# Performance work log

Measured on AMD Instinct MI355X. Metric: run time of the kernel, lower is better.

## Reference

```python
import jax, jax.numpy as jnp
import numpy as np

B, T = 32, 64
STOCH, DETER, HIDDEN = 1024, 4096, 1024
ACT_DIM, EMBED = 128, 1536
MIN_STD = 0.1
EPS = 1e-3  # dreamerv3-torch uses LayerNorm(eps=1e-3)


def _ln(x, g, b):
    m = jnp.mean(x, -1, keepdims=True)
    v = jnp.var(x, -1, keepdims=True)
    return (x - m) * jax.lax.rsqrt(v + EPS) * g + b


def setup_inputs() -> dict:
    key = jax.random.key(0)
    ks = jax.random.split(key, 24)

    def w(k, fan_in, fan_out):
        return jax.random.normal(k, (fan_in, fan_out), jnp.float32) / np.sqrt(fan_in)

    inp = {
        "embed": jax.random.normal(ks[0], (B, T, EMBED), jnp.float32),
        "action": jax.random.normal(ks[1], (B, T, ACT_DIM), jnp.float32),
        "is_first": jnp.zeros((B, T), jnp.bool_),
        "init_deter": jax.random.normal(ks[2], (B, DETER), jnp.float32),
        "init_stoch": jax.random.normal(ks[3], (B, STOCH), jnp.float32),
        "noise_prior": jax.random.normal(ks[4], (B, T, STOCH), jnp.float32),
        "noise_post": jax.random.normal(ks[5], (B, T, STOCH), jnp.float32),
        # _img_in_layers: Linear(stoch+act -> hidden, no bias) + LN + SiLU
        "W_in": w(ks[6], STOCH + ACT_DIM, HIDDEN),
        "g_in": 1.0 + 0.1 * jax.random.normal(ks[7], (HIDDEN,), jnp.float32),
        "b_in": 0.1 * jax.random.normal(ks[8], (HIDDEN,), jnp.float32),
        # GRUCell: Linear(hidden+deter -> 3*deter, no bias) + LN
        "W_gru": w(ks[9], HIDDEN + DETER, 3 * DETER),
        "g_gru": 1.0 + 0.1 * jax.random.normal(ks[10], (3 * DETER,), jnp.float32),
        "b_gru": 0.1 * jax.random.normal(ks[11], (3 * DETER,), jnp.float32),
        # _img_out_layers: Linear(deter -> hidden, no bias) + LN + SiLU
        "W_imgout": w(ks[12], DETER, HIDDEN),
        "g_io": 1.0 + 0.1 * jax.random.normal(ks[13], (HIDDEN,), jnp.float32),
        "b_io": 0.1 * jax.random.normal(ks[14], (HIDDEN,), jnp.float32),
        # _obs_out_layers: Linear(deter+embed -> hidden, no bias) + LN + SiLU
        "W_obsout": w(ks[15], DETER + EMBED, HIDDEN),
        "g_oo": 1.0 + 0.1 * jax.random.normal(ks[16], (HIDDEN,), jnp.float32),
        "b_oo": 0.1 * jax.random.normal(ks[17], (HIDDEN,), jnp.float32),
        # suff-stats layers: Linear(hidden -> 2*stoch) with bias
        "W_ims": w(ks[18], HIDDEN, 2 * STOCH),
        "b_ims": 0.01 * jax.random.normal(ks[19], (2 * STOCH,), jnp.float32),
        "W_obs": w(ks[20], HIDDEN, 2 * STOCH),
        "b_obs": 0.01 * jax.random.normal(ks[21], (2 * STOCH,), jnp.float32),
    }
    return inp


def _observe(embed, action, init_deter, init_stoch, noise_prior, noise_post,
             W_in, g_in, b_in, W_gru, g_gru, b_gru, W_imgout, g_io, b_io,
             W_obsout, g_oo, b_oo, W_ims, b_ims, W_obs, b_obs):
    def suff_stats(h, W, b, noise):
        stats = h @ W + b
        mean, std = jnp.split(stats, 2, -1)
        std = jax.nn.softplus(std) + MIN_STD  # std_act='softplus', mean_act='none'
        return mean, std, mean + std * noise

    def step(carry, xs):
        deter, stoch = carry
        e, a, n_p, n_q = xs
        # img_in: concat(prev_stoch, action) -> Linear -> LN -> SiLU
        x = jax.nn.silu(_ln(jnp.concatenate([stoch, a], -1) @ W_in, g_in, b_in))
        # GRUCell with layernorm (update_bias = -1)
        parts = _ln(jnp.concatenate([x, deter], -1) @ W_gru, g_gru, b_gru)
        reset, cand, update = jnp.split(parts, 3, -1)
        reset = jax.nn.sigmoid(reset)
        cand = jnp.tanh(reset * cand)
        update = jax.nn.sigmoid(update - 1.0)
        deter = update * cand + (1.0 - update) * deter
        # prior (imagination) suff stats + sample
        h_p = jax.nn.silu(_ln(deter @ W_imgout, g_io, b_io))
        mean_p, std_p, stoch_p = suff_stats(h_p, W_ims, b_ims, n_p)
        # posterior (observation) suff stats + sample
        h_q = jax.nn.silu(_ln(jnp.concatenate([deter, e], -1) @ W_obsout, g_oo, b_oo))
        mean_q, std_q, stoch_q = suff_stats(h_q, W_obs, b_obs, n_q)
        out = jnp.concatenate([deter, stoch_q, mean_q, std_q, stoch_p, mean_p, std_p], -1)
        return (deter, stoch_q), out

    xs = (jnp.swapaxes(embed, 0, 1), jnp.swapaxes(action, 0, 1),
          jnp.swapaxes(noise_prior, 0, 1), jnp.swapaxes(noise_post, 0, 1))
    _, outs = jax.lax.scan(step, (init_deter, init_stoch), xs)
    return jnp.swapaxes(outs, 0, 1)  # [B, T, deter + 6*stoch]


def reference(embed, action, is_first, init_deter, init_stoch, noise_prior, noise_post,
              W_in, g_in, b_in, W_gru, g_gru, b_gru, W_imgout, g_io, b_io,
              W_obsout, g_oo, b_oo, W_ims, b_ims, W_obs, b_obs):
    # is_first is all-False and state is given, so the init-mixing branch is never taken
    del is_first
    return _observe(embed, action, init_deter, init_stoch, noise_prior, noise_post,
                    W_in, g_in, b_in, W_gru, g_gru, b_gru, W_imgout, g_io, b_io,
                    W_obsout, g_oo, b_oo, W_ims, b_ims, W_obs, b_obs)
```

## Files before the change

kernel.cpp:

```cpp
#include <hip/hip_runtime.h>
#include <hip/hip_bf16.h>

#define B_ 32
#define T_ 64
#define STOCH_ 1024
#define DETER_ 4096
#define HID_ 1024
#define EMB_ 1536
#define ACTD_ 128
#define GRUK 5120
#define GRUN 12288
#define KC 512
#define LDAP (KC + 8)

typedef __attribute__((ext_vector_type(8))) __bf16 bf16x8;
typedef __attribute__((ext_vector_type(4))) float f32x4;
typedef __attribute__((ext_vector_type(8))) unsigned short u16x8;
typedef __attribute__((ext_vector_type(4))) unsigned short u16x4;

__device__ inline unsigned short f2bf(float f) {
    union { float f; unsigned u; } x; x.f = f;
    unsigned r = x.u + 0x7fffu + ((x.u >> 16) & 1u);
    return (unsigned short)(r >> 16);
}
__device__ inline float sigmoidf_(float v) { return 1.f / (1.f + __expf(-v)); }
__device__ inline float siluf_(float v)    { return v / (1.f + __expf(-v)); }
__device__ inline float softplusf_(float v){ return fmaxf(v, 0.f) + __logf(1.f + __expf(-fabsf(v))); }


__global__ __launch_bounds__(256) void k_pack(const float* __restrict__ W,
                                              unsigned short* __restrict__ dst,
                                              int K, int N) {
    long fid = (long)blockIdx.x * 256 + threadIdx.x;
    long nfr = (long)K * N / 8;
    if (fid >= nfr) return;
    int lane = (int)(fid & 63);
    long tile = fid >> 6;
    int ktiles = K >> 5;
    int k_t = (int)(tile % ktiles);
    int n_t = (int)(tile / ktiles);
    int c = lane & 15, kb = lane >> 4;
    int k0 = k_t * 32 + kb * 8;
    int n = n_t * 16 + c;
    unsigned short v[8];
#pragma unroll
    for (int i = 0; i < 8; i++) v[i] = f2bf(W[(long)(k0 + i) * N + n]);
    *reinterpret_cast<u16x8*>(dst + fid * 8) = *reinterpret_cast<u16x8*>(v);
}

__global__ __launch_bounds__(256) void k_conv(const float* __restrict__ s,
                                              unsigned short* __restrict__ d, long n) {
    long i = ((long)blockIdx.x * 256 + threadIdx.x) * 4;
    if (i >= n) return;
    f32x4 v = *reinterpret_cast<const f32x4*>(s + i);
    unsigned short o[4];
#pragma unroll
    for (int k = 0; k < 4; k++) o[k] = f2bf(v[k]);
    *reinterpret_cast<u16x4*>(d + i) = *reinterpret_cast<u16x4*>(o);
}

__global__ __launch_bounds__(256) void k_copy(const float* __restrict__ s,
                                              float* __restrict__ d, long n) {
    long i = ((long)blockIdx.x * 256 + threadIdx.x) * 4;
    if (i >= n) return;
    *reinterpret_cast<f32x4*>(d + i) = *reinterpret_cast<const f32x4*>(s + i);
}


__device__ inline void ln_stats_prologue(const float* __restrict__ partials, int nslab,
                                         float invN, float* s_mean, float* s_rstd) {
    if (threadIdx.x < 32) {
        int r = threadIdx.x;
        float s = 0.f, q = 0.f;
        for (int j = 0; j < nslab; j++) {
            s += partials[((long)j * 32 + r) * 2];
            q += partials[((long)j * 32 + r) * 2 + 1];
        }
        float m = s * invN;
        float var = q * invN - m * m;
        s_mean[r] = m;
        s_rstd[r] = rsqrtf(var + 1e-3f);
    }
    __syncthreads();
}

__device__ inline void stage_bf16(unsigned short* __restrict__ lds_a,
                                  const unsigned short* __restrict__ src,
                                  int lda, int k0, int cw) {
    for (int e = (int)threadIdx.x * 8; e < 32 * cw; e += 256 * 8) {
        int row = e / cw, col = e - row * cw;
        *reinterpret_cast<u16x8*>(&lds_a[row * LDAP + col]) =
            *reinterpret_cast<const u16x8*>(&src[(long)row * lda + k0 + col]);
    }
}

__device__ inline void stage_lnsilu(unsigned short* __restrict__ lds_a,
                                    const float* __restrict__ raw, int ldr, int colbase,
                                    int k0, int cw,
                                    const float* __restrict__ g, const float* __restrict__ b,
                                    const float* s_mean, const float* s_rstd) {
    for (int e = (int)threadIdx.x * 8; e < 32 * cw; e += 256 * 8) {
        int row = e / cw, col = e - row * cw;
        int kg = k0 + col;
        float m = s_mean[row], rs = s_rstd[row];
        const float* sp = &raw[(long)row * ldr + colbase + kg];
        unsigned short v[8];
#pragma unroll
        for (int i = 0; i < 8; i++) {
            float ln = (sp[i] - m) * rs * g[kg + i] + b[kg + i];
            v[i] = f2bf(siluf_(ln));
        }
        *reinterpret_cast<u16x8*>(&lds_a[row * LDAP + col]) = *reinterpret_cast<u16x8*>(v);
    }
}

__device__ inline void mfma_chunk(const unsigned short* __restrict__ lds_a,
                                  const unsigned short* __restrict__ Bp,
                                  int ntile, long Ktiles, long kt0, int nkt,
                                  int lane, f32x4& acc0, f32x4& acc1) {
    int c = lane & 15, kb = lane >> 4;
    const unsigned short* a0p = &lds_a[c * LDAP + kb * 8];
    const unsigned short* a1p = &lds_a[(16 + c) * LDAP + kb * 8];
    const unsigned short* bp = Bp + ((long)ntile * Ktiles + kt0) * 512 + lane * 8;
    for (int kt = 0; kt < nkt; ++kt) {
        bf16x8 a0 = *reinterpret_cast<const bf16x8*>(a0p + kt * 32);
        bf16x8 a1 = *reinterpret_cast<const bf16x8*>(a1p + kt * 32);
        bf16x8 bv = *reinterpret_cast<const bf16x8*>(bp + (long)kt * 512);
        acc0 = __builtin_amdgcn_mfma_f32_16x16x32_bf16(a0, bv, acc0, 0, 0, 0);
        acc1 = __builtin_amdgcn_mfma_f32_16x16x32_bf16(a1, bv, acc1, 0, 0, 0);
    }
}

__device__ inline void acc_to_lds(float (*s_out)[66], int wave, int lane,
                                  const f32x4& acc0, const f32x4& acc1) {
    int c = lane & 15, rb = lane >> 4;
#pragma unroll
    for (int j = 0; j < 4; j++) {
        s_out[rb * 4 + j][wave * 16 + c] = acc0[j];
        s_out[16 + rb * 4 + j][wave * 16 + c] = acc1[j];
    }
}

__device__ inline void epi_raw(float (*s_out)[66],
                               const float* __restrict__ addin, long addin_ld, int n0_add,
                               float* __restrict__ outp, long out_ld, int n0_out,
                               float* __restrict__ partials, int slab) {
    int row = threadIdx.x >> 3, c8 = (threadIdx.x & 7) * 8;
    float vals[8];
#pragma unroll
    for (int i = 0; i < 8; i++) {
        float v = s_out[row][c8 + i];
        if (addin) v += addin[(long)row * addin_ld + n0_add + c8 + i];
        vals[i] = v;
        s_out[row][c8 + i] = v;
    }
#pragma unroll
    for (int i = 0; i < 8; i++) outp[(long)row * out_ld + n0_out + c8 + i] = vals[i];
    __syncthreads();
    if (threadIdx.x < 32) {
        float s = 0.f, q = 0.f;
        for (int j = 0; j < 64; j++) { float v = s_out[threadIdx.x][j]; s += v; q += v * v; }
        partials[((long)slab * 32 + threadIdx.x) * 2] = s;
        partials[((long)slab * 32 + threadIdx.x) * 2 + 1] = q;
    }
}


__global__ __launch_bounds__(256) void k_x(const unsigned short* __restrict__ Bp,
                                           const unsigned short* __restrict__ stoch_bf16,
                                           const float* __restrict__ A_pre_t,
                                           float* __restrict__ x_raw, float* __restrict__ px) {
    __shared__ __align__(16) unsigned short lds_a[32 * LDAP];
    __shared__ float s_out[32][66];
    int wave = threadIdx.x >> 6, lane = threadIdx.x & 63;
    int ntile = blockIdx.x * 4 + wave;
    f32x4 acc0 = {0.f, 0.f, 0.f, 0.f}, acc1 = {0.f, 0.f, 0.f, 0.f};
    for (int ch = 0; ch < 2; ++ch) {
        __syncthreads();
        stage_bf16(lds_a, stoch_bf16, STOCH_, ch * KC, KC);
        __syncthreads();
        mfma_chunk(lds_a, Bp, ntile, 32, ch * 16, 16, lane, acc0, acc1);
    }
    __syncthreads();
    acc_to_lds(s_out, wave, lane, acc0, acc1);
    __syncthreads();
    epi_raw(s_out, A_pre_t, (long)T_ * 1024, blockIdx.x * 64,
            x_raw, 1024, blockIdx.x * 64, px, blockIdx.x);
}

__global__ __launch_bounds__(256) void k_gru(const unsigned short* __restrict__ Bp,
                                             const float* __restrict__ x_raw,
                                             const float* __restrict__ px,
                                             const float* __restrict__ g_in,
                                             const float* __restrict__ b_in,
                                             const unsigned short* __restrict__ deter_bf16,
                                             float* __restrict__ G_raw, float* __restrict__ pg) {
    __shared__ __align__(16) unsigned short lds_a[32 * LDAP];
    __shared__ float s_out[32][66];
    __shared__ float s_mean[32], s_rstd[32];
    ln_stats_prologue(px, 16, 1.f / 1024.f, s_mean, s_rstd);
    int wave = threadIdx.x >> 6, lane = threadIdx.x & 63;
    int ntile = blockIdx.x * 4 + wave;
    f32x4 acc0 = {0.f, 0.f, 0.f, 0.f}, acc1 = {0.f, 0.f, 0.f, 0.f};
    for (int ch = 0; ch < 10; ++ch) {
        __syncthreads();
        if (ch < 2) stage_lnsilu(lds_a, x_raw, 1024, 0, ch * KC, KC, g_in, b_in, s_mean, s_rstd);
        else        stage_bf16(lds_a, deter_bf16, DETER_, ch * KC - 1024, KC);
        __syncthreads();
        mfma_chunk(lds_a, Bp, ntile, 160, ch * 16, 16, lane, acc0, acc1);
    }
    __syncthreads();
    acc_to_lds(s_out, wave, lane, acc0, acc1);
    __syncthreads();
    epi_raw(s_out, nullptr, 0, 0, G_raw, GRUN, blockIdx.x * 64, pg, blockIdx.x);
}

__global__ __launch_bounds__(256) void k_deter(const float* __restrict__ G_raw,
                                               const float* __restrict__ pg,
                                               const float* __restrict__ g_gru,
                                               const float* __restrict__ b_gru,
                                               float* __restrict__ deter_f32,
                                               unsigned short* __restrict__ deter_bf16,
                                               float* __restrict__ out, int t) {
    __shared__ float s_mean[32], s_rstd[32];
    ln_stats_prologue(pg, 192, 1.f / 12288.f, s_mean, s_rstd);
    int eid = blockIdx.x * 256 + threadIdx.x;
    int b = eid >> 10;
    int j = (eid & 1023) * 4;
    const float* gr = G_raw + (long)b * GRUN;
    f32x4 r4 = *reinterpret_cast<const f32x4*>(gr + j);
    f32x4 c4 = *reinterpret_cast<const f32x4*>(gr + 4096 + j);
    f32x4 u4 = *reinterpret_cast<const f32x4*>(gr + 8192 + j);
    f32x4 d4 = *reinterpret_cast<const f32x4*>(deter_f32 + (long)b * DETER_ + j);
    float m = s_mean[b], rs = s_rstd[b];
    f32x4 nd;
    unsigned short db[4];
#pragma unroll
    for (int i = 0; i < 4; i++) {
        float lr = (r4[i] - m) * rs * g_gru[j + i] + b_gru[j + i];
        float lc = (c4[i] - m) * rs * g_gru[4096 + j + i] + b_gru[4096 + j + i];
        float lu = (u4[i] - m) * rs * g_gru[8192 + j + i] + b_gru[8192 + j + i];
        float reset = sigmoidf_(lr);
        float cand = tanhf(reset * lc);
        float upd = sigmoidf_(lu - 1.f);
        float dn = upd * cand + (1.f - upd) * d4[i];
        nd[i] = dn; db[i] = f2bf(dn);
    }
    *reinterpret_cast<f32x4*>(deter_f32 + (long)b * DETER_ + j) = nd;
    *reinterpret_cast<u16x4*>(deter_bf16 + (long)b * DETER_ + j) = *reinterpret_cast<u16x4*>(db);
    *reinterpret_cast<f32x4*>(out + ((long)(b * T_ + t)) * 10240 + j) = nd;
}

__global__ __launch_bounds__(256) void k_h(const unsigned short* __restrict__ Wio,
                                           const unsigned short* __restrict__ Wood,
                                           const unsigned short* __restrict__ deter_bf16,
                                           const float* __restrict__ E_pre_t,
                                           float* __restrict__ h_raw, float* __restrict__ ph) {
    __shared__ __align__(16) unsigned short lds_a[32 * LDAP];
    __shared__ float s_out[32][66];
    int p = blockIdx.x < 16;
    int bi = blockIdx.x & 15;
    const unsigned short* Bp = p ? Wio : Wood;
    int wave = threadIdx.x >> 6, lane = threadIdx.x & 63;
    int ntile = bi * 4 + wave;
    f32x4 acc0 = {0.f, 0.f, 0.f, 0.f}, acc1 = {0.f, 0.f, 0.f, 0.f};
    for (int ch = 0; ch < 8; ++ch) {
        __syncthreads();
        stage_bf16(lds_a, deter_bf16, DETER_, ch * KC, KC);
        __syncthreads();
        mfma_chunk(lds_a, Bp, ntile, 128, ch * 16, 16, lane, acc0, acc1);
    }
    __syncthreads();
    acc_to_lds(s_out, wave, lane, acc0, acc1);
    __syncthreads();
    epi_raw(s_out, p ? nullptr : E_pre_t, (long)T_ * 1024, bi * 64,
            h_raw, 2048, (p ? 0 : 1024) + bi * 64, ph, blockIdx.x);
}

__global__ __launch_bounds__(256) void k_stats(const unsigned short* __restrict__ Wims,
                                               const unsigned short* __restrict__ Wobs,
                                               const float* __restrict__ h_raw,
                                               const float* __restrict__ ph,
                                               const float* __restrict__ g_io,
                                               const float* __restrict__ b_io,
                                               const float* __restrict__ g_oo,
                                               const float* __restrict__ b_oo,
                                               const float* __restrict__ b_ims,
                                               const float* __restrict__ b_obs,
                                               const float* __restrict__ noise_p,
                                               const float* __restrict__ noise_q,
                                               float* __restrict__ out,
                                               unsigned short* __restrict__ stoch_bf16, int t) {
    __shared__ __align__(16) unsigned short lds_a[32 * LDAP];
    __shared__ float s_out[32][66];
    __shared__ float s_mean[32], s_rstd[32];
    int q = blockIdx.x >= 32;
    int s = blockIdx.x & 31;
    ln_stats_prologue(ph + (q ? 16 * 32 * 2 : 0), 16, 1.f / 1024.f, s_mean, s_rstd);
    const unsigned short* Bp = q ? Wobs : Wims;
    const float* g = q ? g_oo : g_io;
    const float* bb = q ? b_oo : b_io;
    const float* bias = q ? b_obs : b_ims;
    int colbase = q ? 1024 : 0;
    int wave = threadIdx.x >> 6, lane = threadIdx.x & 63;
    int ntile = (wave < 2) ? (s * 2 + wave) : (64 + s * 2 + (wave - 2));
    f32x4 acc0 = {0.f, 0.f, 0.f, 0.f}, acc1 = {0.f, 0.f, 0.f, 0.f};
    for (int ch = 0; ch < 2; ++ch) {
        __syncthreads();
        stage_lnsilu(lds_a, h_raw, 2048, colbase, ch * KC, KC, g, bb, s_mean, s_rstd);
        __syncthreads();
        mfma_chunk(lds_a, Bp, ntile, 32, ch * 16, 16, lane, acc0, acc1);
    }
    __syncthreads();
    int c = lane & 15, rb = lane >> 4;
    float bv = bias[ntile * 16 + c];
#pragma unroll
    for (int j = 0; j < 4; j++) {
        s_out[rb * 4 + j][wave * 16 + c] = acc0[j] + bv;
        s_out[16 + rb * 4 + j][wave * 16 + c] = acc1[j] + bv;
    }
    __syncthreads();
    int r = threadIdx.x >> 3, j0 = (threadIdx.x & 7) * 4;
    const float* noise = q ? noise_q : noise_p;
#pragma unroll
    for (int i = 0; i < 4; i++) {
        int jj = j0 + i;
        float mean = s_out[r][jj];
        float sv = s_out[r][32 + jj];
        float sd = softplusf_(sv) + 0.1f;
        int cg = s * 32 + jj;
        float nz = noise[((long)(r * T_ + t)) * 1024 + cg];
        float st = mean + sd * nz;
        float* orow = out + ((long)(r * T_ + t)) * 10240;
        if (q) {
            orow[4096 + cg] = st; orow[5120 + cg] = mean; orow[6144 + cg] = sd;
            stoch_bf16[(long)r * 1024 + cg] = f2bf(st);
        } else {
            orow[7168 + cg] = st; orow[8192 + cg] = mean; orow[9216 + cg] = sd;
        }
    }
}

__global__ __launch_bounds__(256) void k_prepgemm(const unsigned short* __restrict__ A, int K,
                                                  const unsigned short* __restrict__ Bp,
                                                  float* __restrict__ outp) {
    __shared__ __align__(16) unsigned short lds_a[32 * LDAP];
    __shared__ float s_out[32][66];
    int wave = threadIdx.x >> 6, lane = threadIdx.x & 63;
    int ntile = blockIdx.x * 4 + wave;
    int m0 = blockIdx.y * 32;
    int Ktiles = K >> 5;
    f32x4 acc0 = {0.f, 0.f, 0.f, 0.f}, acc1 = {0.f, 0.f, 0.f, 0.f};
    int nch = (K + KC - 1) / KC;
    for (int ch = 0; ch < nch; ++ch) {
        int cw = K - ch * KC; if (cw > KC) cw = KC;
        __syncthreads();
        stage_bf16(lds_a, A + (long)m0 * K, K, ch * KC, cw);
        __syncthreads();
        mfma_chunk(lds_a, Bp, ntile, Ktiles, ch * 16, cw >> 5, lane, acc0, acc1);
    }
    __syncthreads();
    acc_to_lds(s_out, wave, lane, acc0, acc1);
    __syncthreads();
    int row = threadIdx.x >> 3, c8 = (threadIdx.x & 7) * 8;
#pragma unroll
    for (int i = 0; i < 8; i++)
        outp[(long)(m0 + row) * 1024 + blockIdx.x * 64 + c8 + i] = s_out[row][c8 + i];
}


extern "C" void kernel_launch(void* const* d_in, const int* in_sizes, int n_in,
                              void* d_out, int out_size, void* d_ws, size_t ws_size,
                              hipStream_t stream) {
    const float* embed      = (const float*)d_in[0];
    const float* action     = (const float*)d_in[1];
    const float* init_deter = (const float*)d_in[3];
    const float* init_stoch = (const float*)d_in[4];
    const float* noise_pr   = (const float*)d_in[5];
    const float* noise_po   = (const float*)d_in[6];
    const float* W_in       = (const float*)d_in[7];
    const float* g_in       = (const float*)d_in[8];
    const float* b_in       = (const float*)d_in[9];
    const float* W_gru      = (const float*)d_in[10];
    const float* g_gru      = (const float*)d_in[11];
    const float* b_gru      = (const float*)d_in[12];
    const float* W_io       = (const float*)d_in[13];
    const float* g_io       = (const float*)d_in[14];
    const float* b_io       = (const float*)d_in[15];
    const float* W_oo       = (const float*)d_in[16];
    const float* g_oo       = (const float*)d_in[17];
    const float* b_oo       = (const float*)d_in[18];
    const float* W_ims      = (const float*)d_in[19];
    const float* b_ims      = (const float*)d_in[20];
    const float* W_obs      = (const float*)d_in[21];
    const float* b_obs      = (const float*)d_in[22];
    float* out = (float*)d_out;

    char* ws = (char*)d_ws;
    size_t off = 0;
    auto alloc = [&](size_t bytes) {
        size_t r = off;
        off = (off + bytes + 255) & ~(size_t)255;
        return r;
    };
    unsigned short* pWgru  = (unsigned short*)(ws + alloc((size_t)GRUK * GRUN * 2));
    unsigned short* pWin_s = (unsigned short*)(ws + alloc((size_t)1024 * 1024 * 2));
    unsigned short* pWin_a = (unsigned short*)(ws + alloc((size_t)128 * 1024 * 2));
    unsigned short* pWio   = (unsigned short*)(ws + alloc((size_t)4096 * 1024 * 2));
    unsigned short* pWood  = (unsigned short*)(ws + alloc((size_t)4096 * 1024 * 2));
    unsigned short* pWooe  = (unsigned short*)(ws + alloc((size_t)1536 * 1024 * 2));
    unsigned short* pWims  = (unsigned short*)(ws + alloc((size_t)1024 * 2048 * 2));
    unsigned short* pWobs  = (unsigned short*)(ws + alloc((size_t)1024 * 2048 * 2));
    unsigned short* act_bf = (unsigned short*)(ws + alloc((size_t)2048 * 128 * 2));
    unsigned short* emb_bf = (unsigned short*)(ws + alloc((size_t)2048 * 1536 * 2));
    float* A_pre  = (float*)(ws + alloc((size_t)2048 * 1024 * 4));
    float* E_pre  = (float*)(ws + alloc((size_t)2048 * 1024 * 4));
    float* x_raw  = (float*)(ws + alloc((size_t)32 * 1024 * 4));
    float* G_raw  = (float*)(ws + alloc((size_t)32 * GRUN * 4));
    float* h_raw  = (float*)(ws + alloc((size_t)32 * 2048 * 4));
    float* deterf = (float*)(ws + alloc((size_t)32 * DETER_ * 4));
    unsigned short* deterb = (unsigned short*)(ws + alloc((size_t)32 * DETER_ * 2));
    unsigned short* stochb = (unsigned short*)(ws + alloc((size_t)32 * 1024 * 2));
    float* px = (float*)(ws + alloc((size_t)16 * 32 * 2 * 4));
    float* pg = (float*)(ws + alloc((size_t)192 * 32 * 2 * 4));
    float* ph = (float*)(ws + alloc((size_t)32 * 32 * 2 * 4));
    (void)ws_size; (void)out_size; (void)n_in; (void)in_sizes;

    auto packgrid = [](long K, long N) { return (unsigned)((K * N / 8 + 255) / 256); };

    k_pack<<<packgrid(5120, 12288), 256, 0, stream>>>(W_gru, pWgru, 5120, 12288);
    k_pack<<<packgrid(1024, 1024), 256, 0, stream>>>(W_in, pWin_s, 1024, 1024);
    k_pack<<<packgrid(128, 1024), 256, 0, stream>>>(W_in + (size_t)1024 * 1024, pWin_a, 128, 1024);
    k_pack<<<packgrid(4096, 1024), 256, 0, stream>>>(W_io, pWio, 4096, 1024);
    k_pack<<<packgrid(4096, 1024), 256, 0, stream>>>(W_oo, pWood, 4096, 1024);
    k_pack<<<packgrid(1536, 1024), 256, 0, stream>>>(W_oo + (size_t)4096 * 1024, pWooe, 1536, 1024);
    k_pack<<<packgrid(1024, 2048), 256, 0, stream>>>(W_ims, pWims, 1024, 2048);
    k_pack<<<packgrid(1024, 2048), 256, 0, stream>>>(W_obs, pWobs, 1024, 2048);
    k_conv<<<(2048 * 128 / 4 + 255) / 256, 256, 0, stream>>>(action, act_bf, 2048L * 128);
    k_conv<<<(2048 * 1536 / 4 + 255) / 256, 256, 0, stream>>>(embed, emb_bf, 2048L * 1536);
    k_conv<<<(32 * 1024 / 4 + 255) / 256, 256, 0, stream>>>(init_stoch, stochb, 32L * 1024);
    k_conv<<<(32 * 4096 / 4 + 255) / 256, 256, 0, stream>>>(init_deter, deterb, 32L * 4096);
    k_copy<<<(32 * 4096 / 4 + 255) / 256, 256, 0, stream>>>(init_deter, deterf, 32L * 4096);
    k_prepgemm<<<dim3(16, 64), 256, 0, stream>>>(act_bf, 128, pWin_a, A_pre);
    k_prepgemm<<<dim3(16, 64), 256, 0, stream>>>(emb_bf, 1536, pWooe, E_pre);

    for (int t = 0; t < T_; ++t) {
        k_x<<<16, 256, 0, stream>>>(pWin_s, stochb, A_pre + (size_t)t * 1024, x_raw, px);
        k_gru<<<192, 256, 0, stream>>>(pWgru, x_raw, px, g_in, b_in, deterb, G_raw, pg);
        k_deter<<<128, 256, 0, stream>>>(G_raw, pg, g_gru, b_gru, deterf, deterb, out, t);
        k_h<<<32, 256, 0, stream>>>(pWio, pWood, deterb, E_pre + (size_t)t * 1024, h_raw, ph);
        k_stats<<<64, 256, 0, stream>>>(pWims, pWobs, h_raw, ph, g_io, b_io, g_oo, b_oo,
                                        b_ims, b_obs, noise_pr, noise_po, out, stochb, t);
    }
}
```

Measured before the change: 7.235 ms.

## Hoist prior branch out of recurrence and pipeline GEMMs with async LDS loads

The prior-path computation (img_out layer and prior suff stats) does not feed the recurrence, so it moves out of the per-step loop. Each step's deter is saved to a bf16 buffer, and the prior branch then runs as one batched GEMM over all 2048 rows after the loop. The per-step GEMMs are unified into a templated kernel. It double-buffers A tiles in LDS using global_load_lds with an XOR swizzle, and uses smaller 32-column N tiles so more blocks run. The GRU candidate also switches to a fast exp-based tanh, which trades a little accuracy and adds a 16 MB buffer for the saved deter history.

```diff
diff --git a/kernel.cpp b/kernel.cpp
--- a/kernel.cpp
+++ b/kernel.cpp
@@ -1,17 +1,9 @@
 #include <hip/hip_runtime.h>
 #include <hip/hip_bf16.h>
 
-#define B_ 32
 #define T_ 64
-#define STOCH_ 1024
 #define DETER_ 4096
-#define HID_ 1024
-#define EMB_ 1536
-#define ACTD_ 128
-#define GRUK 5120
 #define GRUN 12288
-#define KC 512
-#define LDAP (KC + 8)
 
 typedef __attribute__((ext_vector_type(8))) __bf16 bf16x8;
 typedef __attribute__((ext_vector_type(4))) float f32x4;
@@ -26,6 +18,19 @@
 __device__ inline float sigmoidf_(float v) { return 1.f / (1.f + __expf(-v)); }
 __device__ inline float siluf_(float v)    { return v / (1.f + __expf(-v)); }
 __device__ inline float softplusf_(float v){ return fmaxf(v, 0.f) + __logf(1.f + __expf(-fabsf(v))); }
+__device__ inline float tanhf_(float v)    { return 2.f / (1.f + __expf(-2.f * v)) - 1.f; }
+
+__device__ inline void barrier_() {
+    asm volatile("" ::: "memory");
+    __builtin_amdgcn_s_barrier();
+    asm volatile("" ::: "memory");
+}
+template <int N> __device__ inline void vmwaitN() {
+    asm volatile("s_waitcnt vmcnt(%0)" :: "i"(N) : "memory");
+}
+__device__ inline void lgkmwait_() {
+    asm volatile("s_waitcnt lgkmcnt(0)" ::: "memory");
+}
 
 
 __global__ __launch_bounds__(256) void k_pack(const float* __restrict__ W,
@@ -67,152 +72,137 @@
 }
 
 
-__device__ inline void ln_stats_prologue(const float* __restrict__ partials, int nslab,
-                                         float invN, float* s_mean, float* s_rstd) {
-    if (threadIdx.x < 32) {
-        int r = threadIdx.x;
-        float s = 0.f, q = 0.f;
-        for (int j = 0; j < nslab; j++) {
-            s += partials[((long)j * 32 + r) * 2];
-            q += partials[((long)j * 32 + r) * 2 + 1];
+template <int CW>
+__device__ inline void stage_glds(unsigned short* chunk, const unsigned short* __restrict__ src,
+                                  long ld, long k0) {
+    constexpr int NI = (32 * CW * 2) / 4096;
+    int wv = (int)threadIdx.x >> 6, lane = (int)threadIdx.x & 63;
+#pragma unroll
+    for (int i = 0; i < NI; ++i) {
+        int obase = (wv * NI + i) << 10;
+        int o = obase + lane * 16;
+        int row = o / (CW * 2);
+        int cb = o - row * (CW * 2);
+        int gb = cb ^ ((row & 7) << 4);
+        const char* ga = (const char*)(src + (long)row * ld + k0) + gb;
+        __builtin_amdgcn_global_load_lds(
+            (const __attribute__((address_space(1))) void*)ga,
+            (__attribute__((address_space(3))) void*)(chunk + (obase >> 1)),
+            16, 0, 0);
+    }
+}
+
+__device__ inline void stage_ln512(unsigned short* chunk, const float* __restrict__ raw,
+                                   int ld, int col0,
+                                   const float* __restrict__ g, const float* __restrict__ b,
+                                   const float* s_mean, const float* s_rstd) {
+    int tid = threadIdx.x;
+#pragma unroll
+    for (int i = 0; i < 8; ++i) {
+        int e = tid * 8 + i * 2048;
+        int row = e >> 9, col = e & 511;
+        float m = s_mean[row], rs = s_rstd[row];
+        const float* sp = raw + (long)row * ld + col0 + col;
+        unsigned short pk[8];
+#pragma unroll
+        for (int j = 0; j < 8; ++j) {
+            float ln = (sp[j] - m) * rs * g[col0 + col + j] + b[col0 + col + j];
+            pk[j] = f2bf(siluf_(ln));
         }
-        float m = s * invN;
-        float var = q * invN - m * m;
-        s_mean[r] = m;
-        s_rstd[r] = rsqrtf(var + 1e-3f);
-    }
-    __syncthreads();
-}
-
-__device__ inline void stage_bf16(unsigned short* __restrict__ lds_a,
-                                  const unsigned short* __restrict__ src,
-                                  int lda, int k0, int cw) {
-    for (int e = (int)threadIdx.x * 8; e < 32 * cw; e += 256 * 8) {
-        int row = e / cw, col = e - row * cw;
-        *reinterpret_cast<u16x8*>(&lds_a[row * LDAP + col]) =
-            *reinterpret_cast<const u16x8*>(&src[(long)row * lda + k0 + col]);
-    }
-}
-
-__device__ inline void stage_lnsilu(unsigned short* __restrict__ lds_a,
-                                    const float* __restrict__ raw, int ldr, int colbase,
-                                    int k0, int cw,
-                                    const float* __restrict__ g, const float* __restrict__ b,
-                                    const float* s_mean, const float* s_rstd) {
-    for (int e = (int)threadIdx.x * 8; e < 32 * cw; e += 256 * 8) {
-        int row = e / cw, col = e - row * cw;
-        int kg = k0 + col;
-        float m = s_mean[row], rs = s_rstd[row];
-        const float* sp = &raw[(long)row * ldr + colbase + kg];
-        unsigned short v[8];
-#pragma unroll
-        for (int i = 0; i < 8; i++) {
-            float ln = (sp[i] - m) * rs * g[kg + i] + b[kg + i];
-            v[i] = f2bf(siluf_(ln));
+        int dcol = col ^ ((row & 7) << 3);
+        *reinterpret_cast<u16x8*>(chunk + row * 512 + dcol) = *reinterpret_cast<u16x8*>(pk);
+    }
+}
+
+template <int CW>
+__device__ inline void mfma_rh(const unsigned short* chunk, int row, int kb,
+                               const unsigned short* __restrict__ bp, f32x4& acc) {
+    constexpr int NKT = CW / 32;
+    const unsigned short* ap = chunk + row * CW;
+    int sw = (row & 7) << 3;
+#pragma unroll
+    for (int kt = 0; kt < NKT; ++kt) {
+        bf16x8 a = *reinterpret_cast<const bf16x8*>(ap + ((kb * 8 + kt * 32) ^ sw));
+        bf16x8 b = *reinterpret_cast<const bf16x8*>(bp + (long)kt * 512);
+        acc = __builtin_amdgcn_mfma_f32_16x16x32_bf16(a, b, acc, 0, 0, 0);
+    }
+}
+
+template <int CW, int NG, int NL>
+__global__ __launch_bounds__(256) void k_gemm32(
+    const unsigned short* __restrict__ Bp, int Ktiles, int ktg0,
+    const unsigned short* __restrict__ srcA, long ldA,
+    const float* __restrict__ lnraw, int lnld,
+    const float* __restrict__ g_ln, const float* __restrict__ b_ln,
+    const float* __restrict__ pstats, int nslab_in,
+    const float* __restrict__ addin, long addin_ld,
+    float* __restrict__ outp, long out_ld,
+    float* __restrict__ partials, long prows)
+{
+    constexpr int NCH = NG + NL;
+    constexpr int NI = (32 * CW * 2) / 4096;
+    __shared__ __align__(16) unsigned short sb[2][32 * CW];
+    __shared__ float s_out[32][34];
+    __shared__ float s_mean[32], s_rstd[32];
+    int tid = threadIdx.x;
+    if (NL > 0) {
+        if (tid < 32) {
+            float s = 0.f, q = 0.f;
+            for (int j = 0; j < nslab_in; ++j) {
+                s += pstats[((long)j * 32 + tid) * 2];
+                q += pstats[((long)j * 32 + tid) * 2 + 1];
+            }
+            float m = s * (1.f / 1024.f);
+            s_mean[tid] = m;
+            s_rstd[tid] = rsqrtf(q * (1.f / 1024.f) - m * m + 1e-3f);
         }
-        *reinterpret_cast<u16x8*>(&lds_a[row * LDAP + col]) = *reinterpret_cast<u16x8*>(v);
-    }
-}
-
-__device__ inline void mfma_chunk(const unsigned short* __restrict__ lds_a,
-                                  const unsigned short* __restrict__ Bp,
-                                  int ntile, long Ktiles, long kt0, int nkt,
-                                  int lane, f32x4& acc0, f32x4& acc1) {
+        __syncthreads();
+    }
+    int rowbase = blockIdx.y * 32;
+    const unsigned short* srcAr = srcA + (long)rowbase * ldA;
+    int lane = tid & 63, wv = tid >> 6;
+    int nt = wv >> 1, rh = wv & 1;
     int c = lane & 15, kb = lane >> 4;
-    const unsigned short* a0p = &lds_a[c * LDAP + kb * 8];
-    const unsigned short* a1p = &lds_a[(16 + c) * LDAP + kb * 8];
-    const unsigned short* bp = Bp + ((long)ntile * Ktiles + kt0) * 512 + lane * 8;
-    for (int kt = 0; kt < nkt; ++kt) {
-        bf16x8 a0 = *reinterpret_cast<const bf16x8*>(a0p + kt * 32);
-        bf16x8 a1 = *reinterpret_cast<const bf16x8*>(a1p + kt * 32);
-        bf16x8 bv = *reinterpret_cast<const bf16x8*>(bp + (long)kt * 512);
-        acc0 = __builtin_amdgcn_mfma_f32_16x16x32_bf16(a0, bv, acc0, 0, 0, 0);
-        acc1 = __builtin_amdgcn_mfma_f32_16x16x32_bf16(a1, bv, acc1, 0, 0, 0);
-    }
-}
-
-__device__ inline void acc_to_lds(float (*s_out)[66], int wave, int lane,
-                                  const f32x4& acc0, const f32x4& acc1) {
-    int c = lane & 15, rb = lane >> 4;
-#pragma unroll
-    for (int j = 0; j < 4; j++) {
-        s_out[rb * 4 + j][wave * 16 + c] = acc0[j];
-        s_out[16 + rb * 4 + j][wave * 16 + c] = acc1[j];
-    }
-}
-
-__device__ inline void epi_raw(float (*s_out)[66],
-                               const float* __restrict__ addin, long addin_ld, int n0_add,
-                               float* __restrict__ outp, long out_ld, int n0_out,
-                               float* __restrict__ partials, int slab) {
-    int row = threadIdx.x >> 3, c8 = (threadIdx.x & 7) * 8;
-    float vals[8];
-#pragma unroll
-    for (int i = 0; i < 8; i++) {
-        float v = s_out[row][c8 + i];
-        if (addin) v += addin[(long)row * addin_ld + n0_add + c8 + i];
-        vals[i] = v;
-        s_out[row][c8 + i] = v;
-    }
-#pragma unroll
-    for (int i = 0; i < 8; i++) outp[(long)row * out_ld + n0_out + c8 + i] = vals[i];
-    __syncthreads();
-    if (threadIdx.x < 32) {
-        float s = 0.f, q = 0.f;
-        for (int j = 0; j < 64; j++) { float v = s_out[threadIdx.x][j]; s += v; q += v * v; }
-        partials[((long)slab * 32 + threadIdx.x) * 2] = s;
-        partials[((long)slab * 32 + threadIdx.x) * 2 + 1] = q;
-    }
-}
-
-
-__global__ __launch_bounds__(256) void k_x(const unsigned short* __restrict__ Bp,
-                                           const unsigned short* __restrict__ stoch_bf16,
-                                           const float* __restrict__ A_pre_t,
-                                           float* __restrict__ x_raw, float* __restrict__ px) {
-    __shared__ __align__(16) unsigned short lds_a[32 * LDAP];
-    __shared__ float s_out[32][66];
-    int wave = threadIdx.x >> 6, lane = threadIdx.x & 63;
-    int ntile = blockIdx.x * 4 + wave;
-    f32x4 acc0 = {0.f, 0.f, 0.f, 0.f}, acc1 = {0.f, 0.f, 0.f, 0.f};
-    for (int ch = 0; ch < 2; ++ch) {
-        __syncthreads();
-        stage_bf16(lds_a, stoch_bf16, STOCH_, ch * KC, KC);
-        __syncthreads();
-        mfma_chunk(lds_a, Bp, ntile, 32, ch * 16, 16, lane, acc0, acc1);
-    }
-    __syncthreads();
-    acc_to_lds(s_out, wave, lane, acc0, acc1);
-    __syncthreads();
-    epi_raw(s_out, A_pre_t, (long)T_ * 1024, blockIdx.x * 64,
-            x_raw, 1024, blockIdx.x * 64, px, blockIdx.x);
-}
-
-__global__ __launch_bounds__(256) void k_gru(const unsigned short* __restrict__ Bp,
-                                             const float* __restrict__ x_raw,
-                                             const float* __restrict__ px,
-                                             const float* __restrict__ g_in,
-                                             const float* __restrict__ b_in,
-                                             const unsigned short* __restrict__ deter_bf16,
-                                             float* __restrict__ G_raw, float* __restrict__ pg) {
-    __shared__ __align__(16) unsigned short lds_a[32 * LDAP];
-    __shared__ float s_out[32][66];
-    __shared__ float s_mean[32], s_rstd[32];
-    ln_stats_prologue(px, 16, 1.f / 1024.f, s_mean, s_rstd);
-    int wave = threadIdx.x >> 6, lane = threadIdx.x & 63;
-    int ntile = blockIdx.x * 4 + wave;
-    f32x4 acc0 = {0.f, 0.f, 0.f, 0.f}, acc1 = {0.f, 0.f, 0.f, 0.f};
-    for (int ch = 0; ch < 10; ++ch) {
-        __syncthreads();
-        if (ch < 2) stage_lnsilu(lds_a, x_raw, 1024, 0, ch * KC, KC, g_in, b_in, s_mean, s_rstd);
-        else        stage_bf16(lds_a, deter_bf16, DETER_, ch * KC - 1024, KC);
-        __syncthreads();
-        mfma_chunk(lds_a, Bp, ntile, 160, ch * 16, 16, lane, acc0, acc1);
-    }
-    __syncthreads();
-    acc_to_lds(s_out, wave, lane, acc0, acc1);
-    __syncthreads();
-    epi_raw(s_out, nullptr, 0, 0, G_raw, GRUN, blockIdx.x * 64, pg, blockIdx.x);
+    int mrow = rh * 16 + c;
+    long ntg = (long)blockIdx.x * 2 + nt;
+    const unsigned short* bbase = Bp + (long)ntg * Ktiles * 512 + lane * 8;
+    f32x4 acc = {0.f, 0.f, 0.f, 0.f};
+    stage_glds<CW>(sb[0], srcAr, ldA, 0);
+    for (int ch = 0; ch < NCH; ++ch) {
+        int nx = ch + 1;
+        if (nx < NG) stage_glds<CW>(sb[nx & 1], srcAr, ldA, (long)nx * CW);
+        else if (nx < NCH) stage_ln512(sb[nx & 1], lnraw, lnld, (nx - NG) * 512,
+                                       g_ln, b_ln, s_mean, s_rstd);
+        if (ch < NG) { if (nx < NG) vmwaitN<NI>(); else vmwaitN<0>(); }
+        if (nx >= NG && nx < NCH) lgkmwait_();
+        barrier_();
+        int kt0 = (ch < NG) ? (ktg0 + ch * (CW / 32)) : ((ch - NG) * 16);
+        mfma_rh<CW>(sb[ch & 1], mrow, kb, bbase + (long)kt0 * 512, acc);
+        barrier_();
+    }
+    __syncthreads();
+#pragma unroll
+    for (int j = 0; j < 4; ++j) s_out[rh * 16 + kb * 4 + j][nt * 16 + c] = acc[j];
+    __syncthreads();
+    int orow = tid >> 3, c4 = (tid & 7) * 4;
+    long rg = rowbase + orow;
+    float v[4]; float s = 0.f, q = 0.f;
+#pragma unroll
+    for (int i = 0; i < 4; ++i) {
+        float x = s_out[orow][c4 + i];
+        if (addin) x += addin[rg * addin_ld + blockIdx.x * 32 + c4 + i];
+        v[i] = x; s += x; q += x * x;
+    }
+#pragma unroll
+    for (int i = 0; i < 4; ++i) outp[rg * out_ld + blockIdx.x * 32 + c4 + i] = v[i];
+    if (partials) {
+#pragma unroll
+        for (int m = 1; m < 8; m <<= 1) { s += __shfl_xor(s, m); q += __shfl_xor(q, m); }
+        if ((tid & 7) == 0) {
+            partials[((long)blockIdx.x * prows + rg) * 2] = s;
+            partials[((long)blockIdx.x * prows + rg) * 2 + 1] = q;
+        }
+    }
 }
 
 __global__ __launch_bounds__(256) void k_deter(const float* __restrict__ G_raw,
@@ -221,10 +211,31 @@
                                                const float* __restrict__ b_gru,
                                                float* __restrict__ deter_f32,
                                                unsigned short* __restrict__ deter_bf16,
+                                               unsigned short* __restrict__ deter_allb,
                                                float* __restrict__ out, int t) {
     __shared__ float s_mean[32], s_rstd[32];
-    ln_stats_prologue(pg, 192, 1.f / 12288.f, s_mean, s_rstd);
-    int eid = blockIdx.x * 256 + threadIdx.x;
+    __shared__ float s_red[2][8][32];
+    int tid = threadIdx.x;
+    {
+        int r = tid & 31, g = tid >> 5;
+        float s = 0.f, q = 0.f;
+        for (int j = g; j < 384; j += 8) {
+            s += pg[((long)j * 32 + r) * 2];
+            q += pg[((long)j * 32 + r) * 2 + 1];
+        }
+        s_red[0][g][r] = s; s_red[1][g][r] = q;
+    }
+    __syncthreads();
+    if (tid < 32) {
+        float s = 0.f, q = 0.f;
+#pragma unroll
+        for (int g = 0; g < 8; ++g) { s += s_red[0][g][tid]; q += s_red[1][g][tid]; }
+        float m = s * (1.f / 12288.f);
+        s_mean[tid] = m;
+        s_rstd[tid] = rsqrtf(q * (1.f / 12288.f) - m * m + 1e-3f);
+    }
+    __syncthreads();
+    int eid = blockIdx.x * 256 + tid;
     int b = eid >> 10;
     int j = (eid & 1023) * 4;
     const float* gr = G_raw + (long)b * GRUN;
@@ -241,131 +252,154 @@
         float lc = (c4[i] - m) * rs * g_gru[4096 + j + i] + b_gru[4096 + j + i];
         float lu = (u4[i] - m) * rs * g_gru[8192 + j + i] + b_gru[8192 + j + i];
         float reset = sigmoidf_(lr);
-        float cand = tanhf(reset * lc);
+        float cand = tanhf_(reset * lc);
         float upd = sigmoidf_(lu - 1.f);
         float dn = upd * cand + (1.f - upd) * d4[i];
         nd[i] = dn; db[i] = f2bf(dn);
     }
     *reinterpret_cast<f32x4*>(deter_f32 + (long)b * DETER_ + j) = nd;
     *reinterpret_cast<u16x4*>(deter_bf16 + (long)b * DETER_ + j) = *reinterpret_cast<u16x4*>(db);
-    *reinterpret_cast<f32x4*>(out + ((long)(b * T_ + t)) * 10240 + j) = nd;
-}
-
-__global__ __launch_bounds__(256) void k_h(const unsigned short* __restrict__ Wio,
-                                           const unsigned short* __restrict__ Wood,
-                                           const unsigned short* __restrict__ deter_bf16,
-                                           const float* __restrict__ E_pre_t,
-                                           float* __restrict__ h_raw, float* __restrict__ ph) {
-    __shared__ __align__(16) unsigned short lds_a[32 * LDAP];
-    __shared__ float s_out[32][66];
-    int p = blockIdx.x < 16;
-    int bi = blockIdx.x & 15;
-    const unsigned short* Bp = p ? Wio : Wood;
-    int wave = threadIdx.x >> 6, lane = threadIdx.x & 63;
-    int ntile = bi * 4 + wave;
-    f32x4 acc0 = {0.f, 0.f, 0.f, 0.f}, acc1 = {0.f, 0.f, 0.f, 0.f};
-    for (int ch = 0; ch < 8; ++ch) {
-        __syncthreads();
-        stage_bf16(lds_a, deter_bf16, DETER_, ch * KC, KC);
-        __syncthreads();
-        mfma_chunk(lds_a, Bp, ntile, 128, ch * 16, 16, lane, acc0, acc1);
-    }
-    __syncthreads();
-    acc_to_lds(s_out, wave, lane, acc0, acc1);
-    __syncthreads();
-    epi_raw(s_out, p ? nullptr : E_pre_t, (long)T_ * 1024, bi * 64,
-            h_raw, 2048, (p ? 0 : 1024) + bi * 64, ph, blockIdx.x);
-}
-
-__global__ __launch_bounds__(256) void k_stats(const unsigned short* __restrict__ Wims,
-                                               const unsigned short* __restrict__ Wobs,
-                                               const float* __restrict__ h_raw,
-                                               const float* __restrict__ ph,
-                                               const float* __restrict__ g_io,
-                                               const float* __restrict__ b_io,
-                                               const float* __restrict__ g_oo,
-                                               const float* __restrict__ b_oo,
-                                               const float* __restrict__ b_ims,
-                                               const float* __restrict__ b_obs,
-                                               const float* __restrict__ noise_p,
-                                               const float* __restrict__ noise_q,
-                                               float* __restrict__ out,
-                                               unsigned short* __restrict__ stoch_bf16, int t) {
-    __shared__ __align__(16) unsigned short lds_a[32 * LDAP];
+    long orow = (long)b * T_ + t;
+    *reinterpret_cast<u16x4*>(deter_allb + orow * DETER_ + j) = *reinterpret_cast<u16x4*>(db);
+    *reinterpret_cast<f32x4*>(out + orow * 10240 + j) = nd;
+}
+
+__global__ __launch_bounds__(256) void k_statsq(
+    const unsigned short* __restrict__ Bp, const float* __restrict__ hq_raw,
+    const float* __restrict__ ph,
+    const float* __restrict__ g_oo, const float* __restrict__ b_oo,
+    const float* __restrict__ bias,
+    const float* __restrict__ noise, float* __restrict__ out,
+    unsigned short* __restrict__ stochb, int t)
+{
+    __shared__ __align__(16) unsigned short sb[2][32 * 512];
     __shared__ float s_out[32][66];
     __shared__ float s_mean[32], s_rstd[32];
-    int q = blockIdx.x >= 32;
-    int s = blockIdx.x & 31;
-    ln_stats_prologue(ph + (q ? 16 * 32 * 2 : 0), 16, 1.f / 1024.f, s_mean, s_rstd);
-    const unsigned short* Bp = q ? Wobs : Wims;
-    const float* g = q ? g_oo : g_io;
-    const float* bb = q ? b_oo : b_io;
-    const float* bias = q ? b_obs : b_ims;
-    int colbase = q ? 1024 : 0;
-    int wave = threadIdx.x >> 6, lane = threadIdx.x & 63;
-    int ntile = (wave < 2) ? (s * 2 + wave) : (64 + s * 2 + (wave - 2));
-    f32x4 acc0 = {0.f, 0.f, 0.f, 0.f}, acc1 = {0.f, 0.f, 0.f, 0.f};
+    int tid = threadIdx.x;
+    if (tid < 32) {
+        float s = 0.f, q = 0.f;
+        for (int j = 0; j < 32; ++j) {
+            s += ph[((long)j * 32 + tid) * 2];
+            q += ph[((long)j * 32 + tid) * 2 + 1];
+        }
+        float m = s * (1.f / 1024.f);
+        s_mean[tid] = m;
+        s_rstd[tid] = rsqrtf(q * (1.f / 1024.f) - m * m + 1e-3f);
+    }
+    __syncthreads();
+    int lane = tid & 63, wv = tid >> 6;
+    int part = wv >> 1, nt = wv & 1;
+    int c = lane & 15, kb = lane >> 4;
+    int s_ = blockIdx.x;
+    long ntg = (long)part * 64 + s_ * 2 + nt;
+    const unsigned short* bbase = Bp + ntg * 32 * 512 + lane * 8;
+    f32x4 acc0 = {0.f,0.f,0.f,0.f}, acc1 = {0.f,0.f,0.f,0.f};
+    stage_ln512(sb[0], hq_raw, 1024, 0, g_oo, b_oo, s_mean, s_rstd);
     for (int ch = 0; ch < 2; ++ch) {
-        __syncthreads();
-        stage_lnsilu(lds_a, h_raw, 2048, colbase, ch * KC, KC, g, bb, s_mean, s_rstd);
-        __syncthreads();
-        mfma_chunk(lds_a, Bp, ntile, 32, ch * 16, 16, lane, acc0, acc1);
-    }
-    __syncthreads();
-    int c = lane & 15, rb = lane >> 4;
-    float bv = bias[ntile * 16 + c];
-#pragma unroll
-    for (int j = 0; j < 4; j++) {
-        s_out[rb * 4 + j][wave * 16 + c] = acc0[j] + bv;
-        s_out[16 + rb * 4 + j][wave * 16 + c] = acc1[j] + bv;
-    }
-    __syncthreads();
-    int r = threadIdx.x >> 3, j0 = (threadIdx.x & 7) * 4;
-    const float* noise = q ? noise_q : noise_p;
-#pragma unroll
-    for (int i = 0; i < 4; i++) {
-        int jj = j0 + i;
-        float mean = s_out[r][jj];
-        float sv = s_out[r][32 + jj];
-        float sd = softplusf_(sv) + 0.1f;
-        int cg = s * 32 + jj;
-        float nz = noise[((long)(r * T_ + t)) * 1024 + cg];
-        float st = mean + sd * nz;
-        float* orow = out + ((long)(r * T_ + t)) * 10240;
-        if (q) {
-            orow[4096 + cg] = st; orow[5120 + cg] = mean; orow[6144 + cg] = sd;
-            stoch_bf16[(long)r * 1024 + cg] = f2bf(st);
-        } else {
-            orow[7168 + cg] = st; orow[8192 + cg] = mean; orow[9216 + cg] = sd;
+        if (ch == 0) stage_ln512(sb[1], hq_raw, 1024, 512, g_oo, b_oo, s_mean, s_rstd);
+        lgkmwait_();
+        barrier_();
+        const unsigned short* bp = bbase + (long)ch * 16 * 512;
+        mfma_rh<512>(sb[ch], c, kb, bp, acc0);
+        mfma_rh<512>(sb[ch], 16 + c, kb, bp, acc1);
+        barrier_();
+    }
+    __syncthreads();
+    float bv = bias[ntg * 16 + c];
+#pragma unroll
+    for (int j = 0; j < 4; ++j) {
+        s_out[kb * 4 + j][part * 32 + nt * 16 + c] = acc0[j] + bv;
+        s_out[16 + kb * 4 + j][part * 32 + nt * 16 + c] = acc1[j] + bv;
+    }
+    __syncthreads();
+    int r = tid >> 3, j0 = (tid & 7) * 4;
+    long orow = (long)r * T_ + t;
+#pragma unroll
+    for (int i = 0; i < 4; ++i) {
+        int j = j0 + i;
+        float mean = s_out[r][j];
+        float sd = softplusf_(s_out[r][32 + j]) + 0.1f;
+        int cg = s_ * 32 + j;
+        float st = mean + sd * noise[orow * 1024 + cg];
+        float* op = out + orow * 10240;
+        op[4096 + cg] = st; op[5120 + cg] = mean; op[6144 + cg] = sd;
+        stochb[r * 1024 + cg] = f2bf(st);
+    }
+}
+
+__global__ __launch_bounds__(256) void k_bstats(
+    const unsigned short* __restrict__ Bp, const unsigned short* __restrict__ h_pb,
+    const float* __restrict__ bias, const float* __restrict__ noise,
+    float* __restrict__ out)
+{
+    __shared__ __align__(16) unsigned short sb[2][32 * 512];
+    __shared__ float s_out[32][66];
+    int tid = threadIdx.x;
+    int lane = tid & 63, wv = tid >> 6;
+    int part = wv >> 1, nt = wv & 1;
+    int c = lane & 15, kb = lane >> 4;
+    int s_ = blockIdx.x, rowbase = blockIdx.y * 32;
+    const unsigned short* A = h_pb + (long)rowbase * 1024;
+    long ntg = (long)part * 64 + s_ * 2 + nt;
+    const unsigned short* bbase = Bp + ntg * 32 * 512 + lane * 8;
+    f32x4 acc0 = {0.f,0.f,0.f,0.f}, acc1 = {0.f,0.f,0.f,0.f};
+    stage_glds<512>(sb[0], A, 1024, 0);
+    for (int ch = 0; ch < 2; ++ch) {
+        if (ch == 0) { stage_glds<512>(sb[1], A, 1024, 512); vmwaitN<8>(); }
+        else vmwaitN<0>();
+        barrier_();
+        const unsigned short* bp = bbase + (long)ch * 16 * 512;
+        mfma_rh<512>(sb[ch], c, kb, bp, acc0);
+        mfma_rh<512>(sb[ch], 16 + c, kb, bp, acc1);
+        barrier_();
+    }
+    __syncthreads();
+    float bv = bias[ntg * 16 + c];
+#pragma unroll
+    for (int j = 0; j < 4; ++j) {
+        s_out[kb * 4 + j][part * 32 + nt * 16 + c] = acc0[j] + bv;
+        s_out[16 + kb * 4 + j][part * 32 + nt * 16 + c] = acc1[j] + bv;
+    }
+    __syncthreads();
+    int r = tid >> 3, j0 = (tid & 7) * 4;
+    long orow = rowbase + r;
+#pragma unroll
+    for (int i = 0; i < 4; ++i) {
+        int j = j0 + i;
+        float mean = s_out[r][j];
+        float sd = softplusf_(s_out[r][32 + j]) + 0.1f;
+        int cg = s_ * 32 + j;
+        float st = mean + sd * noise[orow * 1024 + cg];
+        float* op = out + orow * 10240;
+        op[7168 + cg] = st; op[8192 + cg] = mean; op[9216 + cg] = sd;
+    }
+}
+
+__global__ __launch_bounds__(256) void k_bfin(const float* __restrict__ hp_raw,
+                                              const float* __restrict__ pbh,
+                                              const float* __restrict__ g_io,
+                                              const float* __restrict__ b_io,
+                                              unsigned short* __restrict__ h_pb) {
+    int row = blockIdx.x * 8 + ((int)threadIdx.x >> 5);
+    int l = threadIdx.x & 31;
+    float s = pbh[((long)l * 2048 + row) * 2];
+    float q = pbh[((long)l * 2048 + row) * 2 + 1];
+#pragma unroll
+    for (int m = 16; m; m >>= 1) { s += __shfl_xor(s, m, 32); q += __shfl_xor(q, m, 32); }
+    float mn = s * (1.f / 1024.f);
+    float rs = rsqrtf(q * (1.f / 1024.f) - mn * mn + 1e-3f);
+#pragma unroll
+    for (int i = 0; i < 8; ++i) {
+        int col = i * 128 + l * 4;
+        f32x4 v = *reinterpret_cast<const f32x4*>(hp_raw + (long)row * 1024 + col);
+        unsigned short pk[4];
+#pragma unroll
+        for (int j = 0; j < 4; ++j) {
+            float ln = (v[j] - mn) * rs * g_io[col + j] + b_io[col + j];
+            pk[j] = f2bf(siluf_(ln));
         }
-    }
-}
-
-__global__ __launch_bounds__(256) void k_prepgemm(const unsigned short* __restrict__ A, int K,
-                                                  const unsigned short* __restrict__ Bp,
-                                                  float* __restrict__ outp) {
-    __shared__ __align__(16) unsigned short lds_a[32 * LDAP];
-    __shared__ float s_out[32][66];
-    int wave = threadIdx.x >> 6, lane = threadIdx.x & 63;
-    int ntile = blockIdx.x * 4 + wave;
-    int m0 = blockIdx.y * 32;
-    int Ktiles = K >> 5;
-    f32x4 acc0 = {0.f, 0.f, 0.f, 0.f}, acc1 = {0.f, 0.f, 0.f, 0.f};
-    int nch = (K + KC - 1) / KC;
-    for (int ch = 0; ch < nch; ++ch) {
-        int cw = K - ch * KC; if (cw > KC) cw = KC;
-        __syncthreads();
-        stage_bf16(lds_a, A + (long)m0 * K, K, ch * KC, cw);
-        __syncthreads();
-        mfma_chunk(lds_a, Bp, ntile, Ktiles, ch * 16, cw >> 5, lane, acc0, acc1);
-    }
-    __syncthreads();
-    acc_to_lds(s_out, wave, lane, acc0, acc1);
-    __syncthreads();
-    int row = threadIdx.x >> 3, c8 = (threadIdx.x & 7) * 8;
-#pragma unroll
-    for (int i = 0; i < 8; i++)
-        outp[(long)(m0 + row) * 1024 + blockIdx.x * 64 + c8 + i] = s_out[row][c8 + i];
+        *reinterpret_cast<u16x4*>(h_pb + (long)row * 1024 + col) = *reinterpret_cast<u16x4*>(pk);
+    }
 }
 
 
@@ -403,7 +437,7 @@
         off = (off + bytes + 255) & ~(size_t)255;
         return r;
     };
-    unsigned short* pWgru  = (unsigned short*)(ws + alloc((size_t)GRUK * GRUN * 2));
+    unsigned short* pWgru  = (unsigned short*)(ws + alloc((size_t)5120 * 12288 * 2));
     unsigned short* pWin_s = (unsigned short*)(ws + alloc((size_t)1024 * 1024 * 2));
     unsigned short* pWin_a = (unsigned short*)(ws + alloc((size_t)128 * 1024 * 2));
     unsigned short* pWio   = (unsigned short*)(ws + alloc((size_t)4096 * 1024 * 2));
@@ -417,13 +451,17 @@
     float* E_pre  = (float*)(ws + alloc((size_t)2048 * 1024 * 4));
     float* x_raw  = (float*)(ws + alloc((size_t)32 * 1024 * 4));
     float* G_raw  = (float*)(ws + alloc((size_t)32 * GRUN * 4));
-    float* h_raw  = (float*)(ws + alloc((size_t)32 * 2048 * 4));
+    float* hq_raw = (float*)(ws + alloc((size_t)32 * 1024 * 4));
     float* deterf = (float*)(ws + alloc((size_t)32 * DETER_ * 4));
-    unsigned short* deterb = (unsigned short*)(ws + alloc((size_t)32 * DETER_ * 2));
+    unsigned short* deterb     = (unsigned short*)(ws + alloc((size_t)32 * DETER_ * 2));
+    unsigned short* deter_allb = (unsigned short*)(ws + alloc((size_t)2048 * DETER_ * 2));
     unsigned short* stochb = (unsigned short*)(ws + alloc((size_t)32 * 1024 * 2));
-    float* px = (float*)(ws + alloc((size_t)16 * 32 * 2 * 4));
-    float* pg = (float*)(ws + alloc((size_t)192 * 32 * 2 * 4));
-    float* ph = (float*)(ws + alloc((size_t)32 * 32 * 2 * 4));
+    float* hp_raw = (float*)(ws + alloc((size_t)2048 * 1024 * 4));
+    unsigned short* h_pb = (unsigned short*)(ws + alloc((size_t)2048 * 1024 * 2));
+    float* px  = (float*)(ws + alloc((size_t)32 * 32 * 2 * 4));
+    float* pg  = (float*)(ws + alloc((size_t)384 * 32 * 2 * 4));
+    float* ph  = (float*)(ws + alloc((size_t)32 * 32 * 2 * 4));
+    float* pbh = (float*)(ws + alloc((size_t)32 * 2048 * 2 * 4));
     (void)ws_size; (void)out_size; (void)n_in; (void)in_sizes;
 
     auto packgrid = [](long K, long N) { return (unsigned)((K * N / 8 + 255) / 256); };
@@ -441,15 +479,32 @@
     k_conv<<<(32 * 1024 / 4 + 255) / 256, 256, 0, stream>>>(init_stoch, stochb, 32L * 1024);
     k_conv<<<(32 * 4096 / 4 + 255) / 256, 256, 0, stream>>>(init_deter, deterb, 32L * 4096);
     k_copy<<<(32 * 4096 / 4 + 255) / 256, 256, 0, stream>>>(init_deter, deterf, 32L * 4096);
-    k_prepgemm<<<dim3(16, 64), 256, 0, stream>>>(act_bf, 128, pWin_a, A_pre);
-    k_prepgemm<<<dim3(16, 64), 256, 0, stream>>>(emb_bf, 1536, pWooe, E_pre);
+    k_gemm32<128, 1, 0><<<dim3(32, 64), 256, 0, stream>>>(
+        pWin_a, 4, 0, act_bf, 128, nullptr, 0, nullptr, nullptr, nullptr, 0,
+        nullptr, 0, A_pre, 1024, nullptr, 0);
+    k_gemm32<512, 3, 0><<<dim3(32, 64), 256, 0, stream>>>(
+        pWooe, 48, 0, emb_bf, 1536, nullptr, 0, nullptr, nullptr, nullptr, 0,
+        nullptr, 0, E_pre, 1024, nullptr, 0);
 
     for (int t = 0; t < T_; ++t) {
-        k_x<<<16, 256, 0, stream>>>(pWin_s, stochb, A_pre + (size_t)t * 1024, x_raw, px);
-        k_gru<<<192, 256, 0, stream>>>(pWgru, x_raw, px, g_in, b_in, deterb, G_raw, pg);
-        k_deter<<<128, 256, 0, stream>>>(G_raw, pg, g_gru, b_gru, deterf, deterb, out, t);
-        k_h<<<32, 256, 0, stream>>>(pWio, pWood, deterb, E_pre + (size_t)t * 1024, h_raw, ph);
-        k_stats<<<64, 256, 0, stream>>>(pWims, pWobs, h_raw, ph, g_io, b_io, g_oo, b_oo,
-                                        b_ims, b_obs, noise_pr, noise_po, out, stochb, t);
-    }
-}
+        k_gemm32<512, 2, 0><<<dim3(32, 1), 256, 0, stream>>>(
+            pWin_s, 32, 0, stochb, 1024, nullptr, 0, nullptr, nullptr, nullptr, 0,
+            A_pre + (size_t)t * 1024, (long)T_ * 1024, x_raw, 1024, px, 32);
+        k_gemm32<512, 8, 2><<<dim3(384, 1), 256, 0, stream>>>(
+            pWgru, 160, 32, deterb, 4096, x_raw, 1024, g_in, b_in, px, 32,
+            nullptr, 0, G_raw, GRUN, pg, 32);
+        k_deter<<<128, 256, 0, stream>>>(G_raw, pg, g_gru, b_gru, deterf, deterb,
+                                         deter_allb, out, t);
+        k_gemm32<512, 8, 0><<<dim3(32, 1), 256, 0, stream>>>(
+            pWood, 128, 0, deterb, 4096, nullptr, 0, nullptr, nullptr, nullptr, 0,
+            E_pre + (size_t)t * 1024, (long)T_ * 1024, hq_raw, 1024, ph, 32);
+        k_statsq<<<32, 256, 0, stream>>>(pWobs, hq_raw, ph, g_oo, b_oo, b_obs,
+                                         noise_po, out, stochb, t);
+    }
+
+    k_gemm32<512, 8, 0><<<dim3(32, 64), 256, 0, stream>>>(
+        pWio, 128, 0, deter_allb, 4096, nullptr, 0, nullptr, nullptr, nullptr, 0,
+        nullptr, 0, hp_raw, 1024, pbh, 2048);
+    k_bfin<<<256, 256, 0, stream>>>(hp_raw, pbh, g_io, b_io, h_pb);
+    k_bstats<<<dim3(32, 64), 256, 0, stream>>>(pWims, h_pb, b_ims, noise_pr, out);
+}
```

New measurement: 8.699 ms. 20.2% more time.
